# Kernel tuning notes

Hardware: AMD Instinct MI355X
Metric: run time of the kernel (lower is better)

## Reference

```python
import jax, jax.numpy as jnp
import numpy as np

B, N, NC = 16, 102000, 35        # batch, raw YOLOv7@1280 predictions, num classes
IMG = 1280                        # input image size
CONF_THRESH = 0.25
IOU_THRESH = 0.45
PRE_TOPK = 1024                   # candidates kept before IoU suppression (yolov7 max_nms analogue)
MAX_DET = 300                     # padded detections per image (yolov7 max_det)


def setup_inputs() -> dict:
    key = jax.random.key(0)
    kxy, kwh, kobj, kcls = jax.random.split(key, 4)
    xy = jax.random.uniform(kxy, (B, N, 2), dtype=jnp.float32) * IMG        # box centers in pixels
    wh = jax.random.uniform(kwh, (B, N, 2), dtype=jnp.float32) * 96.0 + 4.0  # box sizes
    obj = jax.random.uniform(kobj, (B, N, 1), dtype=jnp.float32)            # objectness
    cls = jax.random.uniform(kcls, (B, N, NC), dtype=jnp.float32)           # class scores
    pred = jnp.concatenate([xy, wh, obj, cls], axis=-1)  # [B, N, 5+NC]
    return {"pred": pred}


def _xywh2xyxy(xywh):
    xy, wh = xywh[..., :2], xywh[..., 2:4]
    return jnp.concatenate([xy - wh * 0.5, xy + wh * 0.5], axis=-1)


def _iou_matrix(b):
    # b: [K, 4] xyxy -> [K, K] pairwise IoU
    area = jnp.clip(b[:, 2] - b[:, 0], 0.0) * jnp.clip(b[:, 3] - b[:, 1], 0.0)
    lt = jnp.maximum(b[:, None, :2], b[None, :, :2])
    rb = jnp.minimum(b[:, None, 2:], b[None, :, 2:])
    wh = jnp.clip(rb - lt, 0.0)
    inter = wh[..., 0] * wh[..., 1]
    return inter / (area[:, None] + area[None, :] - inter + 1e-7)


def _nms_single(boxes, scores, cls_id):
    # boxes: [N,4] xyxy, scores: [N] (0 where below conf thresh), cls_id: [N] float
    s, idx = jax.lax.top_k(scores, PRE_TOPK)
    b = boxes[idx]
    c = cls_id[idx]
    iou = _iou_matrix(b)              # [K, K]
    valid = s > 0.0
    ar = jnp.arange(PRE_TOPK)

    def body(suppressed, i):
        keep_i = valid[i] & ~suppressed[i]
        suppressed = suppressed | (keep_i & (iou[i] > IOU_THRESH) & (ar > i))
        return suppressed, keep_i

    _, keep = jax.lax.scan(body, jnp.zeros(PRE_TOPK, bool), ar)
    final = jnp.where(keep, s, 0.0)
    fs, fidx = jax.lax.top_k(final, MAX_DET)
    # [MAX_DET, 6] = x1, y1, x2, y2, conf, cls (conf==0 rows are padding)
    return jnp.concatenate([b[fidx], fs[:, None], c[fidx][:, None]], axis=-1)


def reference(pred):
    # yolov7 non_max_suppression, class-agnostic, best-class per box
    boxes = _xywh2xyxy(pred[..., :4])                    # [B, N, 4]
    obj = pred[..., 4]                                   # [B, N]
    cls_scores = pred[..., 5:] * obj[..., None]          # obj_conf * cls_conf
    conf = jnp.max(cls_scores, axis=-1)                  # [B, N]
    cls_id = jnp.argmax(cls_scores, axis=-1).astype(pred.dtype)
    cand = (obj > CONF_THRESH) & (conf > CONF_THRESH)    # candidate filter
    scores = jnp.where(cand, conf, 0.0)
    return jax.vmap(_nms_single)(boxes, scores, cls_id)  # [B, MAX_DET, 6]
```

## Files before the change

kernel.cpp:

```cpp
#include <hip/hip_runtime.h>
#include <stdint.h>

#define BB 16
#define NN 102000
#define NCLS 35
#define RSTRIDE 40
#define PRE 1024
#define CAP 2048
#define MAXDET 300
#define NBUCK 4096
#define CONF_T 0.25f
#define IOU_T 0.45f
#define BUCK_BASE 0x3E800000u
#define HI_BUCK 3584u
#define HI_BITS 0x3F600000u
#define GL_CAP 16384
#define GCNT_STRIDE 64

#define SCORES_OFF ((size_t)0)
#define SCORES_BYTES ((size_t)BB * NN * 4)
#define GCNT_OFF (SCORES_OFF + SCORES_BYTES)
#define GCNT_BYTES ((size_t)BB * GCNT_STRIDE * 4)
#define BOXES_OFF (GCNT_OFF + GCNT_BYTES)
#define BOXES_BYTES ((size_t)BB * PRE * 16)
#define SVAL_OFF (BOXES_OFF + BOXES_BYTES)
#define SVAL_BYTES ((size_t)BB * PRE * 4)
#define CLS_OFF (SVAL_OFF + SVAL_BYTES)
#define CLS_BYTES ((size_t)BB * PRE * 4)
#define MASK_OFF (CLS_OFF + CLS_BYTES)
#define MASK_BYTES ((size_t)BB * PRE * 16 * 8)
#define GLIST_OFF (MASK_OFF + MASK_BYTES)
#define GLIST_BYTES ((size_t)BB * GL_CAP * 8)

__device__ __forceinline__ int KS(int i) { return i + (i >> 4); }
#define CAPP (CAP + (CAP >> 4))

__global__ __launch_bounds__(256) void k_score(const float* __restrict__ pred,
                                               float* __restrict__ scores,
                                               unsigned int* __restrict__ gcnt,
                                               unsigned long long* __restrict__ glist) {
    __shared__ unsigned long long wbuf[4 * 64];
    __shared__ unsigned int wcnt[4], woff[4];
    __shared__ unsigned int sBase;
    int b = blockIdx.y, tid = threadIdx.x;
    int lane = tid & 63, w = tid >> 6;
    int sub = lane & 7, rg = lane >> 3;
    int rowBase = blockIdx.x * 256 + w * 8 + rg;
    unsigned int wtotal = 0u;
#pragma unroll
    for (int p = 0; p < 8; ++p) {
        int row = rowBase + p * 32;
        bool rv = row < NN;
        const float4* rp = (const float4*)(pred + ((size_t)b * NN + row) * RSTRIDE);
        float4 va = make_float4(0.0f, 0.0f, 0.0f, 0.0f);
        float4 vb = make_float4(0.0f, 0.0f, 0.0f, 0.0f);
        if (rv) va = rp[1 + sub];
        if (rv && sub == 0) vb = rp[9];
        float f0 = (sub == 0) ? va.y : va.x;
        float lm = fmaxf(fmaxf(f0, va.y), fmaxf(va.z, va.w));
        lm = fmaxf(lm, fmaxf(fmaxf(vb.x, vb.y), fmaxf(vb.z, vb.w)));
        lm = fmaxf(lm, __shfl_xor(lm, 1));
        lm = fmaxf(lm, __shfl_xor(lm, 2));
        lm = fmaxf(lm, __shfl_xor(lm, 4));
        float obj = __shfl(va.x, lane & ~7);
        float conf = lm * obj;
        float score = (obj > CONF_T && conf > CONF_T) ? conf : 0.0f;
        unsigned int bits = __float_as_uint(score);
        if (sub == 0 && rv) scores[(size_t)b * NN + row] = score;
        bool want = (sub == 0) && rv && (bits >= HI_BITS) && (score > 0.0f);
        unsigned long long m = __ballot(want);
        if (want) {
            unsigned int off = wtotal + (unsigned int)__popcll(m & ((1ull << lane) - 1ull));
            wbuf[w * 64 + off] = ((unsigned long long)bits << 32) |
                                 (unsigned int)(~(unsigned int)row);
        }
        wtotal += (unsigned int)__popcll(m);
    }
    if (lane == 0) wcnt[w] = wtotal;
    __syncthreads();
    if (tid == 0) {
        unsigned int acc = 0;
        for (int k = 0; k < 4; ++k) { woff[k] = acc; acc += wcnt[k]; }
        sBase = acc ? atomicAdd(&gcnt[b * GCNT_STRIDE], acc) : 0u;
    }
    __syncthreads();
    for (unsigned int i = (unsigned int)lane; i < wtotal; i += 64u) {
        unsigned int pos = sBase + woff[w] + i;
        if (pos < GL_CAP) glist[(size_t)b * GL_CAP + pos] = wbuf[w * 64 + i];
    }
}

__global__ __launch_bounds__(1024) void k_sort(const float* __restrict__ scores,
                                               const unsigned int* __restrict__ gcnt,
                                               const unsigned long long* __restrict__ glist,
                                               const float* __restrict__ pred,
                                               float4* __restrict__ boxesWS,
                                               float* __restrict__ svalWS,
                                               float* __restrict__ clsWS) {
    __shared__ int sA[1024], sB[1024];
    __shared__ unsigned int hh[512];
    __shared__ unsigned int fh[NBUCK];
    __shared__ int cutSh;
    __shared__ unsigned long long keys[CAPP];
    __shared__ unsigned int nloc;
    int b = blockIdx.x, tid = threadIdx.x;
    unsigned int gn = gcnt[b * GCNT_STRIDE];
    if (tid == 0) { cutSh = -1; nloc = 0u; }
    if (tid < 512) hh[tid] = 0u;
    for (int k = tid; k < CAP; k += 1024) keys[KS(k)] = 0ull;
    __syncthreads();
    const unsigned long long* gl = glist + (size_t)b * GL_CAP;
    bool fast = (gn <= (unsigned int)GL_CAP);
    if (fast) {
        for (unsigned int it = tid; it < gn; it += 1024u) {
            unsigned int bits = (unsigned int)(gl[it] >> 32);
            unsigned int bk = (bits - BUCK_BASE) >> 12;
            if (bk > NBUCK - 1u) bk = NBUCK - 1u;
            atomicAdd(&hh[bk - HI_BUCK], 1u);
        }
        __syncthreads();
        if (tid < 512) sA[tid] = (int)hh[tid];
        __syncthreads();
        int* src = sA; int* dst = sB;
        for (int off = 1; off < 512; off <<= 1) {
            if (tid < 512) {
                int x = src[tid];
                if (tid + off < 512) x += src[tid + off];
                dst[tid] = x;
            }
            __syncthreads();
            int* t_ = src; src = dst; dst = t_;
        }
        if (tid < 512) {
            int suf = src[tid];
            int nx = (tid + 1 < 512) ? src[tid + 1] : 0;
            if (suf >= PRE && nx < PRE) cutSh = (int)HI_BUCK + tid;
        }
        __syncthreads();
    }
    int cut = cutSh;
    if (fast && cut >= (int)HI_BUCK) {
        for (unsigned int it = tid; it < gn; it += 1024u) {
            unsigned long long key = gl[it];
            unsigned int bits = (unsigned int)(key >> 32);
            unsigned int bk = (bits - BUCK_BASE) >> 12;
            if (bk > NBUCK - 1u) bk = NBUCK - 1u;
            if ((int)bk >= cut) {
                unsigned int pos = atomicAdd(&nloc, 1u);
                if (pos < CAP) keys[KS((int)pos)] = key;
            }
        }
    } else {
        for (int k = tid; k < NBUCK; k += 1024) fh[k] = 0u;
        __syncthreads();
        const float* sb = scores + (size_t)b * NN;
        for (int it = tid; it < NN; it += 1024) {
            float s = sb[it];
            if (s > 0.0f) {
                unsigned int bits = __float_as_uint(s);
                unsigned int bk = (bits - BUCK_BASE) >> 12;
                if (bk > NBUCK - 1u) bk = NBUCK - 1u;
                atomicAdd(&fh[bk], 1u);
            }
        }
        __syncthreads();
        int h0 = fh[4 * tid + 0], h1 = fh[4 * tid + 1];
        int h2 = fh[4 * tid + 2], h3 = fh[4 * tid + 3];
        if (tid == 0) cutSh = 0;
        sA[tid] = h0 + h1 + h2 + h3;
        __syncthreads();
        int* src = sA; int* dst = sB;
        for (int off = 1; off < 1024; off <<= 1) {
            int x = src[tid];
            if (tid + off < 1024) x += src[tid + off];
            dst[tid] = x;
            __syncthreads();
            int* t_ = src; src = dst; dst = t_;
        }
        int nxt = (tid + 1 < 1024) ? src[tid + 1] : 0;
        int s3 = h3 + nxt;
        int s2 = h2 + s3;
        int s1 = h1 + s2;
        int s0 = h0 + s1;
        if (s0 >= PRE && s1 < PRE) cutSh = 4 * tid + 0;
        if (s1 >= PRE && s2 < PRE) cutSh = 4 * tid + 1;
        if (s2 >= PRE && s3 < PRE) cutSh = 4 * tid + 2;
        if (s3 >= PRE && nxt < PRE) cutSh = 4 * tid + 3;
        __syncthreads();
        unsigned int ccut = (unsigned int)cutSh;
        const float4* sb4 = (const float4*)sb;
        for (int it = tid; it < NN / 4; it += 1024) {
            float4 s4 = sb4[it];
            float sv[4] = {s4.x, s4.y, s4.z, s4.w};
#pragma unroll
            for (int u = 0; u < 4; ++u) {
                float s = sv[u];
                if (s > 0.0f) {
                    unsigned int bits = __float_as_uint(s);
                    unsigned int bk = (bits - BUCK_BASE) >> 12;
                    if (bk > NBUCK - 1u) bk = NBUCK - 1u;
                    if (bk >= ccut) {
                        unsigned int pos = atomicAdd(&nloc, 1u);
                        unsigned int idx = (unsigned int)(it * 4 + u);
                        if (pos < CAP)
                            keys[KS((int)pos)] = ((unsigned long long)bits << 32) |
                                                 (unsigned int)(~idx);
                    }
                }
            }
        }
    }
    __syncthreads();

    for (int k = 2; k <= CAP; k <<= 1) {
        for (int j = k >> 1; j > 0; j >>= 1) {
            int p = ((tid & ~(j - 1)) << 1) | (tid & (j - 1));
            int q = p | j;
            int pp = KS(p), qq = KS(q);
            unsigned long long a = keys[pp], c = keys[qq];
            bool desc = (p & k) == 0;
            bool sw = desc ? (a < c) : (a > c);
            if (sw) { keys[pp] = c; keys[qq] = a; }
            __syncthreads();
        }
    }

    unsigned long long key = keys[KS(tid)];
    unsigned int bits = (unsigned int)(key >> 32);
    unsigned int idx = ~(unsigned int)key;
    float sc = __uint_as_float(bits);
    if (bits == 0u || idx >= NN) { idx = 0; sc = 0.0f; }
    const float4* row = (const float4*)(pred + ((size_t)b * NN + idx) * RSTRIDE);
    float4 r0 = row[0];
    float4 r1 = row[1];
    float obj = r1.x;
    float best = r1.y * obj; int bj = 0;
    float p1 = r1.z * obj; if (p1 > best) { best = p1; bj = 1; }
    float p2 = r1.w * obj; if (p2 > best) { best = p2; bj = 2; }
#pragma unroll
    for (int kk = 2; kk <= 9; ++kk) {
        float4 r = row[kk];
        int base = (kk - 2) * 4 + 3;
        float q0 = r.x * obj; if (q0 > best) { best = q0; bj = base + 0; }
        float q1 = r.y * obj; if (q1 > best) { best = q1; bj = base + 1; }
        float q2 = r.z * obj; if (q2 > best) { best = q2; bj = base + 2; }
        float q3 = r.w * obj; if (q3 > best) { best = q3; bj = base + 3; }
    }
    float hx = r0.z * 0.5f;
    float hy = r0.w * 0.5f;
    boxesWS[b * PRE + tid] = make_float4(r0.x - hx, r0.y - hy, r0.x + hx, r0.y + hy);
    svalWS[b * PRE + tid] = sc;
    clsWS[b * PRE + tid] = (float)bj;
}

__global__ __launch_bounds__(256) void k_mask(const float4* __restrict__ boxesWS,
                                              const float* __restrict__ svalWS,
                                              unsigned long long* __restrict__ maskC) {
    __shared__ float bx1[PRE], by1[PRE], bx2[PRE], by2[PRE], bar[PRE], bsv[PRE];
    int b = blockIdx.y, tid = threadIdx.x;
    for (int i = tid; i < PRE; i += 256) {
        float4 bx = boxesWS[b * PRE + i];
        bx1[i] = bx.x; by1[i] = bx.y; bx2[i] = bx.z; by2[i] = bx.w;
        float aw = fmaxf(bx.z - bx.x, 0.0f);
        float ah = fmaxf(bx.w - bx.y, 0.0f);
        bar[i] = aw * ah;
        bsv[i] = svalWS[b * PRE + i];
    }
    __syncthreads();
    int j = blockIdx.x * 4 + (tid >> 6);
    int lane = tid & 63;
    float jx1 = bx1[j], jy1 = by1[j], jx2 = bx2[j], jy2 = by2[j], ja = bar[j];
    unsigned long long* out = maskC + ((size_t)b * PRE + j) * 16;
    for (int c = 0; c < 16; ++c) {
        unsigned long long word = 0ull;
        if (c * 64 < j) {
            int i = c * 64 + lane;
            bool bit = false;
            if (i < j && bsv[i] > 0.0f) {
                float ltx = fmaxf(bx1[i], jx1), lty = fmaxf(by1[i], jy1);
                float rbx = fminf(bx2[i], jx2), rby = fminf(by2[i], jy2);
                float wx = fmaxf(rbx - ltx, 0.0f);
                float wy = fmaxf(rby - lty, 0.0f);
                float inter = wx * wy;
                float denom = ((bar[i] + ja) - inter) + 1e-7f;
                bit = (inter / denom) > IOU_T;
            }
            word = __ballot(bit);
        }
        if (lane == 0) out[c] = word;
    }
}

__global__ __launch_bounds__(1024) void k_nms_out(const float4* __restrict__ boxesWS,
                                                  const float* __restrict__ svalWS,
                                                  const float* __restrict__ clsWS,
                                                  const unsigned long long* __restrict__ maskC,
                                                  float* __restrict__ out) {
    __shared__ unsigned long long supp[16];
    __shared__ int lastch;
    __shared__ int wtot[16], woff[17];
    int b = blockIdx.x, tid = threadIdx.x;
    int lane = tid & 63, w = tid >> 6;
    unsigned long long cm[16];
    const unsigned long long* mrow = maskC + ((size_t)b * PRE + tid) * 16;
#pragma unroll
    for (int k = 0; k < 16; ++k) cm[k] = mrow[k];
    float sv = svalWS[b * PRE + tid];
    if (tid < 16) supp[tid] = 0ull;
    if (tid == 0) lastch = -1;
    __syncthreads();
    for (int it = 0; it < PRE + 2; ++it) {
        bool nb = false;
#pragma unroll
        for (int k = 0; k < 16; ++k) nb |= ((cm[k] & ~supp[k]) != 0ull);
        unsigned long long word = __ballot(nb);
        __syncthreads();
        if (lane == 0) {
            if (word != supp[w]) lastch = it;
            supp[w] = word;
        }
        __syncthreads();
        if (lastch != it) break;
    }
    bool keep = (sv > 0.0f) && !((supp[w] >> lane) & 1ull);
    unsigned long long km = __ballot(keep);
    int lp = __popcll(km & ((lane == 0) ? 0ull : ((1ull << lane) - 1ull)));
    if (lane == 0) wtot[w] = __popcll(km);
    __syncthreads();
    if (tid == 0) {
        int acc = 0;
        for (int k = 0; k < 16; ++k) { woff[k] = acc; acc += wtot[k]; }
        woff[16] = acc;
    }
    __syncthreads();
    int K = woff[16];
    int keptExcl = woff[w] + lp;
    int slot = keep ? keptExcl : (K + (tid - keptExcl));
    if (slot < MAXDET) {
        float4 bx = boxesWS[b * PRE + tid];
        float cv = clsWS[b * PRE + tid];
        float* o = out + ((size_t)b * MAXDET + slot) * 6;
        o[0] = bx.x; o[1] = bx.y; o[2] = bx.z; o[3] = bx.w;
        o[4] = keep ? sv : 0.0f;
        o[5] = cv;
    }
}

extern "C" void kernel_launch(void* const* d_in, const int* in_sizes, int n_in,
                              void* d_out, int out_size, void* d_ws, size_t ws_size,
                              hipStream_t stream) {
    const float* pred = (const float*)d_in[0];
    float* out = (float*)d_out;
    char* ws = (char*)d_ws;
    float* scores = (float*)(ws + SCORES_OFF);
    unsigned int* gcnt = (unsigned int*)(ws + GCNT_OFF);
    float4* boxesWS = (float4*)(ws + BOXES_OFF);
    float* svalWS = (float*)(ws + SVAL_OFF);
    float* clsWS = (float*)(ws + CLS_OFF);
    unsigned long long* maskC = (unsigned long long*)(ws + MASK_OFF);
    unsigned long long* glist = (unsigned long long*)(ws + GLIST_OFF);

    hipMemsetAsync(ws + GCNT_OFF, 0, GCNT_BYTES, stream);
    k_score<<<dim3((NN + 255) / 256, BB), 256, 0, stream>>>(pred, scores, gcnt, glist);
    k_sort<<<BB, 1024, 0, stream>>>(scores, gcnt, glist, pred,
                                    boxesWS, svalWS, clsWS);
    k_mask<<<dim3(PRE / 4, BB), 256, 0, stream>>>(boxesWS, svalWS, maskC);
    k_nms_out<<<BB, 1024, 0, stream>>>(boxesWS, svalWS, clsWS, maskC, out);
}
```

Measured before the change: 418.5 us.

## Drop scores buffer, compute one row per thread, recompute scores in fallback

Removes the dense per-row scores array from the workspace. The scoring kernel now assigns one row per thread, loading all nine float4s itself instead of splitting a row across 8 lanes with shuffles, and appends candidates straight to the global list without the LDS staging buffer. The rare fallback path in k_sort now recomputes scores from pred, which costs far more reads when it is taken. k_mask moves to 1024-thread blocks. The score kernel's reads are less coalesced per instruction, but it drops about 6.5MB of score writes.

```diff
diff --git a/kernel.cpp b/kernel.cpp
--- a/kernel.cpp
+++ b/kernel.cpp
@@ -17,9 +17,7 @@
 #define GL_CAP 16384
 #define GCNT_STRIDE 64
 
-#define SCORES_OFF ((size_t)0)
-#define SCORES_BYTES ((size_t)BB * NN * 4)
-#define GCNT_OFF (SCORES_OFF + SCORES_BYTES)
+#define GCNT_OFF ((size_t)0)
 #define GCNT_BYTES ((size_t)BB * GCNT_STRIDE * 4)
 #define BOXES_OFF (GCNT_OFF + GCNT_BYTES)
 #define BOXES_BYTES ((size_t)BB * PRE * 16)
@@ -35,63 +33,66 @@
 __device__ __forceinline__ int KS(int i) { return i + (i >> 4); }
 #define CAPP (CAP + (CAP >> 4))
 
+__device__ __forceinline__ float row_score(const float* __restrict__ pred,
+                                           int b, int row) {
+    const float4* rp = (const float4*)(pred + ((size_t)b * NN + row) * RSTRIDE);
+    float4 v1 = rp[1];
+    float4 v2 = rp[2];
+    float4 v3 = rp[3];
+    float4 v4 = rp[4];
+    float4 v5 = rp[5];
+    float4 v6 = rp[6];
+    float4 v7 = rp[7];
+    float4 v8 = rp[8];
+    float4 v9 = rp[9];
+    float obj = v1.x;
+    float m0 = fmaxf(fmaxf(v1.y, v1.z), v1.w);
+    float m2 = fmaxf(fmaxf(v2.x, v2.y), fmaxf(v2.z, v2.w));
+    float m3 = fmaxf(fmaxf(v3.x, v3.y), fmaxf(v3.z, v3.w));
+    float m4 = fmaxf(fmaxf(v4.x, v4.y), fmaxf(v4.z, v4.w));
+    float m5 = fmaxf(fmaxf(v5.x, v5.y), fmaxf(v5.z, v5.w));
+    float m6 = fmaxf(fmaxf(v6.x, v6.y), fmaxf(v6.z, v6.w));
+    float m7 = fmaxf(fmaxf(v7.x, v7.y), fmaxf(v7.z, v7.w));
+    float m8 = fmaxf(fmaxf(v8.x, v8.y), fmaxf(v8.z, v8.w));
+    float m9 = fmaxf(fmaxf(v9.x, v9.y), fmaxf(v9.z, v9.w));
+    float mc = fmaxf(fmaxf(fmaxf(m0, m2), fmaxf(m3, m4)),
+                     fmaxf(fmaxf(m5, m6), fmaxf(m7, fmaxf(m8, m9))));
+    float conf = mc * obj;
+    return (obj > CONF_T && conf > CONF_T) ? conf : 0.0f;
+}
+
 __global__ __launch_bounds__(256) void k_score(const float* __restrict__ pred,
-                                               float* __restrict__ scores,
                                                unsigned int* __restrict__ gcnt,
                                                unsigned long long* __restrict__ glist) {
-    __shared__ unsigned long long wbuf[4 * 64];
-    __shared__ unsigned int wcnt[4], woff[4];
+    __shared__ unsigned int sWaveCnt[4];
     __shared__ unsigned int sBase;
     int b = blockIdx.y, tid = threadIdx.x;
+    int row = blockIdx.x * 256 + tid;
+    float score = 0.0f;
+    if (row < NN) score = row_score(pred, b, row);
+    unsigned int bits = __float_as_uint(score);
+    bool want = (score > 0.0f) && (bits >= HI_BITS);
+    unsigned long long m = __ballot(want);
     int lane = tid & 63, w = tid >> 6;
-    int sub = lane & 7, rg = lane >> 3;
-    int rowBase = blockIdx.x * 256 + w * 8 + rg;
-    unsigned int wtotal = 0u;
-#pragma unroll
-    for (int p = 0; p < 8; ++p) {
-        int row = rowBase + p * 32;
-        bool rv = row < NN;
-        const float4* rp = (const float4*)(pred + ((size_t)b * NN + row) * RSTRIDE);
-        float4 va = make_float4(0.0f, 0.0f, 0.0f, 0.0f);
-        float4 vb = make_float4(0.0f, 0.0f, 0.0f, 0.0f);
-        if (rv) va = rp[1 + sub];
-        if (rv && sub == 0) vb = rp[9];
-        float f0 = (sub == 0) ? va.y : va.x;
-        float lm = fmaxf(fmaxf(f0, va.y), fmaxf(va.z, va.w));
-        lm = fmaxf(lm, fmaxf(fmaxf(vb.x, vb.y), fmaxf(vb.z, vb.w)));
-        lm = fmaxf(lm, __shfl_xor(lm, 1));
-        lm = fmaxf(lm, __shfl_xor(lm, 2));
-        lm = fmaxf(lm, __shfl_xor(lm, 4));
-        float obj = __shfl(va.x, lane & ~7);
-        float conf = lm * obj;
-        float score = (obj > CONF_T && conf > CONF_T) ? conf : 0.0f;
-        unsigned int bits = __float_as_uint(score);
-        if (sub == 0 && rv) scores[(size_t)b * NN + row] = score;
-        bool want = (sub == 0) && rv && (bits >= HI_BITS) && (score > 0.0f);
-        unsigned long long m = __ballot(want);
-        if (want) {
-            unsigned int off = wtotal + (unsigned int)__popcll(m & ((1ull << lane) - 1ull));
-            wbuf[w * 64 + off] = ((unsigned long long)bits << 32) |
-                                 (unsigned int)(~(unsigned int)row);
-        }
-        wtotal += (unsigned int)__popcll(m);
-    }
-    if (lane == 0) wcnt[w] = wtotal;
+    if (lane == 0) sWaveCnt[w] = (unsigned int)__popcll(m);
     __syncthreads();
     if (tid == 0) {
-        unsigned int acc = 0;
-        for (int k = 0; k < 4; ++k) { woff[k] = acc; acc += wcnt[k]; }
-        sBase = acc ? atomicAdd(&gcnt[b * GCNT_STRIDE], acc) : 0u;
-    }
-    __syncthreads();
-    for (unsigned int i = (unsigned int)lane; i < wtotal; i += 64u) {
-        unsigned int pos = sBase + woff[w] + i;
-        if (pos < GL_CAP) glist[(size_t)b * GL_CAP + pos] = wbuf[w * 64 + i];
-    }
-}
-
-__global__ __launch_bounds__(1024) void k_sort(const float* __restrict__ scores,
-                                               const unsigned int* __restrict__ gcnt,
+        unsigned int tot = sWaveCnt[0] + sWaveCnt[1] + sWaveCnt[2] + sWaveCnt[3];
+        sBase = tot ? atomicAdd(&gcnt[b * GCNT_STRIDE], tot) : 0u;
+    }
+    __syncthreads();
+    if (want) {
+        unsigned int pos = sBase;
+        for (int k = 0; k < w; ++k) pos += sWaveCnt[k];
+        pos += (unsigned int)__popcll(m & ((1ull << lane) - 1ull));
+        if (pos < GL_CAP)
+            glist[(size_t)b * GL_CAP + pos] =
+                ((unsigned long long)bits << 32) |
+                (unsigned int)(~(unsigned int)row);
+    }
+}
+
+__global__ __launch_bounds__(1024) void k_sort(const unsigned int* __restrict__ gcnt,
                                                const unsigned long long* __restrict__ glist,
                                                const float* __restrict__ pred,
                                                float4* __restrict__ boxesWS,
@@ -153,9 +154,8 @@
     } else {
         for (int k = tid; k < NBUCK; k += 1024) fh[k] = 0u;
         __syncthreads();
-        const float* sb = scores + (size_t)b * NN;
         for (int it = tid; it < NN; it += 1024) {
-            float s = sb[it];
+            float s = row_score(pred, b, it);
             if (s > 0.0f) {
                 unsigned int bits = __float_as_uint(s);
                 unsigned int bk = (bits - BUCK_BASE) >> 12;
@@ -188,24 +188,17 @@
         if (s3 >= PRE && nxt < PRE) cutSh = 4 * tid + 3;
         __syncthreads();
         unsigned int ccut = (unsigned int)cutSh;
-        const float4* sb4 = (const float4*)sb;
-        for (int it = tid; it < NN / 4; it += 1024) {
-            float4 s4 = sb4[it];
-            float sv[4] = {s4.x, s4.y, s4.z, s4.w};
-#pragma unroll
-            for (int u = 0; u < 4; ++u) {
-                float s = sv[u];
-                if (s > 0.0f) {
-                    unsigned int bits = __float_as_uint(s);
-                    unsigned int bk = (bits - BUCK_BASE) >> 12;
-                    if (bk > NBUCK - 1u) bk = NBUCK - 1u;
-                    if (bk >= ccut) {
-                        unsigned int pos = atomicAdd(&nloc, 1u);
-                        unsigned int idx = (unsigned int)(it * 4 + u);
-                        if (pos < CAP)
-                            keys[KS((int)pos)] = ((unsigned long long)bits << 32) |
-                                                 (unsigned int)(~idx);
-                    }
+        for (int it = tid; it < NN; it += 1024) {
+            float s = row_score(pred, b, it);
+            if (s > 0.0f) {
+                unsigned int bits = __float_as_uint(s);
+                unsigned int bk = (bits - BUCK_BASE) >> 12;
+                if (bk > NBUCK - 1u) bk = NBUCK - 1u;
+                if (bk >= ccut) {
+                    unsigned int pos = atomicAdd(&nloc, 1u);
+                    if (pos < CAP)
+                        keys[KS((int)pos)] = ((unsigned long long)bits << 32) |
+                                             (unsigned int)(~(unsigned int)it);
                 }
             }
         }
@@ -253,12 +246,12 @@
     clsWS[b * PRE + tid] = (float)bj;
 }
 
-__global__ __launch_bounds__(256) void k_mask(const float4* __restrict__ boxesWS,
-                                              const float* __restrict__ svalWS,
-                                              unsigned long long* __restrict__ maskC) {
+__global__ __launch_bounds__(1024) void k_mask(const float4* __restrict__ boxesWS,
+                                               const float* __restrict__ svalWS,
+                                               unsigned long long* __restrict__ maskC) {
     __shared__ float bx1[PRE], by1[PRE], bx2[PRE], by2[PRE], bar[PRE], bsv[PRE];
     int b = blockIdx.y, tid = threadIdx.x;
-    for (int i = tid; i < PRE; i += 256) {
+    for (int i = tid; i < PRE; i += 1024) {
         float4 bx = boxesWS[b * PRE + i];
         bx1[i] = bx.x; by1[i] = bx.y; bx2[i] = bx.z; by2[i] = bx.w;
         float aw = fmaxf(bx.z - bx.x, 0.0f);
@@ -267,7 +260,7 @@
         bsv[i] = svalWS[b * PRE + i];
     }
     __syncthreads();
-    int j = blockIdx.x * 4 + (tid >> 6);
+    int j = blockIdx.x * 16 + (tid >> 6);
     int lane = tid & 63;
     float jx1 = bx1[j], jy1 = by1[j], jx2 = bx2[j], jy2 = by2[j], ja = bar[j];
     unsigned long long* out = maskC + ((size_t)b * PRE + j) * 16;
@@ -352,7 +345,6 @@
     const float* pred = (const float*)d_in[0];
     float* out = (float*)d_out;
     char* ws = (char*)d_ws;
-    float* scores = (float*)(ws + SCORES_OFF);
     unsigned int* gcnt = (unsigned int*)(ws + GCNT_OFF);
     float4* boxesWS = (float4*)(ws + BOXES_OFF);
     float* svalWS = (float*)(ws + SVAL_OFF);
@@ -361,9 +353,8 @@
     unsigned long long* glist = (unsigned long long*)(ws + GLIST_OFF);
 
     hipMemsetAsync(ws + GCNT_OFF, 0, GCNT_BYTES, stream);
-    k_score<<<dim3((NN + 255) / 256, BB), 256, 0, stream>>>(pred, scores, gcnt, glist);
-    k_sort<<<BB, 1024, 0, stream>>>(scores, gcnt, glist, pred,
-                                    boxesWS, svalWS, clsWS);
-    k_mask<<<dim3(PRE / 4, BB), 256, 0, stream>>>(boxesWS, svalWS, maskC);
+    k_score<<<dim3((NN + 255) / 256, BB), 256, 0, stream>>>(pred, gcnt, glist);
+    k_sort<<<BB, 1024, 0, stream>>>(gcnt, glist, pred, boxesWS, svalWS, clsWS);
+    k_mask<<<dim3(PRE / 16, BB), 1024, 0, stream>>>(boxesWS, svalWS, maskC);
     k_nms_out<<<BB, 1024, 0, stream>>>(boxesWS, svalWS, clsWS, maskC, out);
 }
```

Result: faster. 402.9 us (-3.7%).
